# Performance work log

Hardware: AMD Instinct MI355X
Metric: run time of the kernel (lower is better)

Reference implementation:

```python
import jax, jax.numpy as jnp
import numpy as np

EPS = 1e-15
NODE_SIZE = 200000
NUM_TYPES = 4
EMBED_DIM = 128
B = 131072
W_POS = 5
W_NEG = 10


def setup_inputs() -> dict:
    key = jax.random.key(0)
    k1, k2, k3, k4, k5, k6 = jax.random.split(key, 6)
    start_node = jax.random.randint(k1, (B, 1), 0, NODE_SIZE)
    pos_samples = jax.random.randint(k2, (B, W_POS), 0, NODE_SIZE)
    neg_samples = jax.random.randint(k3, (B, W_NEG), 0, NODE_SIZE)
    node_types = jax.random.randint(k4, (NODE_SIZE,), 0, NUM_TYPES).astype(jnp.int32)
    start_embeds = jax.random.normal(k5, (NODE_SIZE, EMBED_DIM), dtype=jnp.float32)
    end_embeds = jax.random.normal(k6, (NODE_SIZE, NUM_TYPES, EMBED_DIM), dtype=jnp.float32)
    return {
        'start_embeds': start_embeds,
        'end_embeds': end_embeds,
        'start_node': start_node,
        'pos_samples': pos_samples,
        'neg_samples': neg_samples,
        'node_types': node_types,
    }


def reference(start_embeds, end_embeds, start_node, pos_samples, neg_samples, node_types):
    # start_node: [B,1]; pos_samples: [B,W]; neg_samples: [B,N]
    start_emb = start_embeds[start_node]            # [B,1,D]
    node_type = node_types[start_node]              # [B,1]
    pos_emb = end_embeds[pos_samples, node_type]    # [B,W,D] (node_type broadcasts over W)
    neg_emb = end_embeds[neg_samples, node_type]    # [B,N,D]
    pos_dot = jnp.sum(start_emb * pos_emb, axis=-1)  # [B,W]
    neg_dot = jnp.sum(start_emb * neg_emb, axis=-1)  # [B,N]
    pos_prob = jax.nn.sigmoid(pos_dot)
    neg_prob = jax.nn.sigmoid(neg_dot)
    loss = (-jnp.mean(jnp.log(pos_prob + EPS), axis=1)
            - jnp.mean(jnp.log(1.0 - neg_prob + EPS), axis=1))  # [B]
    return loss
```

## Files before the change

kernel.cpp:

```cpp
#include <hip/hip_runtime.h>
#include <math.h>

#define EPS 1e-15f
#define D 128
#define NTYPES 4

__global__ __launch_bounds__(256) void mp2v_kernel(
    const float* __restrict__ start_embeds,
    const float* __restrict__ end_embeds,
    const int* __restrict__ start_node,
    const int* __restrict__ pos_samples,
    const int* __restrict__ neg_samples,
    const int* __restrict__ node_types,
    float* __restrict__ out,
    int nrows)
{
    const int lane = threadIdx.x & 63;
    const int half = lane >> 5;
    const int m    = lane & 31;
    const int row  = blockIdx.x * (blockDim.x >> 6) + (threadIdx.x >> 6);
    if (row >= nrows) return;

    const int snode = start_node[row];
    const int t     = node_types[snode];

    int myidx = 0;
    if (lane < 5)        myidx = pos_samples[row * 5 + lane];
    else if (lane < 15)  myidx = neg_samples[row * 10 + (lane - 5)];

    const float4 s4 = ((const float4*)(start_embeds + (size_t)snode * D))[m];

    float4 e4[8];
#pragma unroll
    for (int i = 0; i < 8; ++i) {
        int src = 2 * i + half;
        if (src > 14) src = 14;
        const int idx = __shfl(myidx, src);
        e4[i] = ((const float4*)(end_embeds + ((size_t)idx * NTYPES + t) * D))[m];
    }

    float posAcc = 0.0f, negAcc = 0.0f;
#pragma unroll
    for (int i = 0; i < 8; ++i) {
        const float p0 = __fmul_rn(e4[i].x, s4.x);
        const float p1 = __fmul_rn(e4[i].y, s4.y);
        const float p2 = __fmul_rn(e4[i].z, s4.z);
        const float p3 = __fmul_rn(e4[i].w, s4.w);
        float p = __fadd_rn(__fadd_rn(p0, p1), __fadd_rn(p2, p3));
        p = __fadd_rn(p, __shfl_xor(p, 1));
        p = __fadd_rn(p, __shfl_xor(p, 2));
        p = __fadd_rn(p, __shfl_xor(p, 4));
        p = __fadd_rn(p, __shfl_xor(p, 8));
        p = __fadd_rn(p, __shfl_xor(p, 16));

        const float pr = 1.0f / (1.0f + expf(-p));
        const int  s     = 2 * i + half;
        const bool isPos = (s < 5);
        const bool valid = (s < 15);
        const float arg = isPos ? pr : (1.0f - pr);
        const float lg  = logf(arg + EPS);
        posAcc += (isPos && valid) ? lg : 0.0f;
        negAcc += (!isPos && valid) ? lg : 0.0f;
    }

    posAcc += __shfl_xor(posAcc, 32);
    negAcc += __shfl_xor(negAcc, 32);

    if (lane == 0)
        out[row] = -(posAcc / 5.0f) - (negAcc / 10.0f);
}

extern "C" void kernel_launch(void* const* d_in, const int* in_sizes, int n_in,
                              void* d_out, int out_size, void* d_ws, size_t ws_size,
                              hipStream_t stream) {
    const float* start_embeds = (const float*)d_in[0];
    const float* end_embeds   = (const float*)d_in[1];
    const int*   start_node   = (const int*)d_in[2];
    const int*   pos_samples  = (const int*)d_in[3];
    const int*   neg_samples  = (const int*)d_in[4];
    const int*   node_types   = (const int*)d_in[5];
    float* out = (float*)d_out;

    const int nrows = out_size;
    const int wavesPerBlock = 256 / 64;
    const int blocks = (nrows + wavesPerBlock - 1) / wavesPerBlock;
    mp2v_kernel<<<blocks, 256, 0, stream>>>(start_embeds, end_embeds, start_node,
                                            pos_samples, neg_samples, node_types,
                                            out, nrows);
}
```

Baseline: 642.8 us.

## Make kernel persistent with software-pipelined gathers across rows

New measurement: 653.2 us. No clear change (+1.6%).

```diff
diff --git a/kernel.cpp b/kernel.cpp
--- a/kernel.cpp
+++ b/kernel.cpp
@@ -4,6 +4,8 @@
 #define EPS 1e-15f
 #define D 128
 #define NTYPES 4
+#define WPB 4
+#define NBLOCKS 2048
 
 __global__ __launch_bounds__(256) void mp2v_kernel(
     const float* __restrict__ start_embeds,
@@ -18,56 +20,97 @@
     const int lane = threadIdx.x & 63;
     const int half = lane >> 5;
     const int m    = lane & 31;
-    const int row  = blockIdx.x * (blockDim.x >> 6) + (threadIdx.x >> 6);
-    if (row >= nrows) return;
+    const int wid  = blockIdx.x * WPB + (threadIdx.x >> 6);
+    const int nw   = gridDim.x * WPB;
 
-    const int snode = start_node[row];
-    const int t     = node_types[snode];
+    if (wid >= nrows) return;
+    const int iters = (nrows - 1 - wid) / nw + 1;
 
-    int myidx = 0;
-    if (lane < 5)        myidx = pos_samples[row * 5 + lane];
-    else if (lane < 15)  myidx = neg_samples[row * 10 + (lane - 5)];
+#define ROWN(n) (wid + (n) * nw)
 
-    const float4 s4 = ((const float4*)(start_embeds + (size_t)snode * D))[m];
+#define STAGE_X(n, sn, mi)                                          \
+    {   int r_ = ROWN(n); if (r_ >= nrows) r_ = nrows - 1;          \
+        sn = start_node[r_];                                        \
+        mi = 0;                                                     \
+        if (lane < 5)       mi = pos_samples[r_ * 5 + lane];        \
+        else if (lane < 15) mi = neg_samples[r_ * 10 + (lane - 5)]; }
 
-    float4 e4[8];
-#pragma unroll
-    for (int i = 0; i < 8; ++i) {
-        int src = 2 * i + half;
-        if (src > 14) src = 14;
-        const int idx = __shfl(myidx, src);
-        e4[i] = ((const float4*)(end_embeds + ((size_t)idx * NTYPES + t) * D))[m];
+#define STAGE_Z(sn, mi, tt, e4, s4)                                 \
+    {   s4 = ((const float4*)(start_embeds + (size_t)(sn) * D))[m]; \
+        _Pragma("unroll")                                           \
+        for (int i_ = 0; i_ < 8; ++i_) {                            \
+            int src_ = 2 * i_ + half; if (src_ > 14) src_ = 14;     \
+            const int idx_ = __shfl((mi), src_);                    \
+            e4[i_] = ((const float4*)(end_embeds +                  \
+                     ((size_t)idx_ * NTYPES + (tt)) * D))[m];       \
+        }                                                           }
+
+#define STAGE_C(n, e4, s4)                                          \
+    {   float posAcc = 0.0f, negAcc = 0.0f;                         \
+        _Pragma("unroll")                                           \
+        for (int i_ = 0; i_ < 8; ++i_) {                            \
+            const float p0 = __fmul_rn(e4[i_].x, s4.x);             \
+            const float p1 = __fmul_rn(e4[i_].y, s4.y);             \
+            const float p2 = __fmul_rn(e4[i_].z, s4.z);             \
+            const float p3 = __fmul_rn(e4[i_].w, s4.w);             \
+            float p = __fadd_rn(__fadd_rn(p0, p1), __fadd_rn(p2, p3)); \
+            p = __fadd_rn(p, __shfl_xor(p, 1));                     \
+            p = __fadd_rn(p, __shfl_xor(p, 2));                     \
+            p = __fadd_rn(p, __shfl_xor(p, 4));                     \
+            p = __fadd_rn(p, __shfl_xor(p, 8));                     \
+            p = __fadd_rn(p, __shfl_xor(p, 16));                    \
+            const float pr = 1.0f / (1.0f + expf(-p));              \
+            const int  s_    = 2 * i_ + half;                       \
+            const bool isPos = (s_ < 5);                            \
+            const bool valid = (s_ < 15);                           \
+            const float arg = isPos ? pr : (1.0f - pr);             \
+            const float lg  = logf(arg + EPS);                      \
+            posAcc += (isPos && valid) ? lg : 0.0f;                 \
+            negAcc += (!isPos && valid) ? lg : 0.0f;                \
+        }                                                           \
+        posAcc += __shfl_xor(posAcc, 32);                           \
+        negAcc += __shfl_xor(negAcc, 32);                           \
+        if (lane == 0)                                              \
+            out[ROWN(n)] = -(posAcc / 5.0f) - (negAcc / 10.0f);     }
+
+    int sn0, mi0, t0;
+    int sn1, mi1, t1;
+    int sn2, mi2, t2;
+    int sn3, mi3;
+    float4 eA[8], eB[8];
+    float4 sA, sB;
+
+    STAGE_X(0, sn0, mi0);
+    STAGE_X(1, sn1, mi1);
+    STAGE_X(2, sn2, mi2);
+    t0 = node_types[sn0];
+    t1 = node_types[sn1];
+    STAGE_Z(sn0, mi0, t0, eA, sA);
+
+    int n = 0;
+    for (; n + 1 < iters; n += 2) {
+        STAGE_X(n + 3, sn3, mi3);
+        t2 = node_types[sn2];
+        STAGE_Z(sn1, mi1, t1, eB, sB);
+        STAGE_C(n, eA, sA);
+        sn1 = sn2; mi1 = mi2; t1 = t2;
+        sn2 = sn3; mi2 = mi3;
+
+        STAGE_X(n + 4, sn3, mi3);
+        t2 = node_types[sn2];
+        if (n + 2 < iters) STAGE_Z(sn1, mi1, t1, eA, sA);
+        STAGE_C(n + 1, eB, sB);
+        sn1 = sn2; mi1 = mi2; t1 = t2;
+        sn2 = sn3; mi2 = mi3;
+    }
+    if (n < iters) {
+        STAGE_C(n, eA, sA);
     }
 
-    float posAcc = 0.0f, negAcc = 0.0f;
-#pragma unroll
-    for (int i = 0; i < 8; ++i) {
-        const float p0 = __fmul_rn(e4[i].x, s4.x);
-        const float p1 = __fmul_rn(e4[i].y, s4.y);
-        const float p2 = __fmul_rn(e4[i].z, s4.z);
-        const float p3 = __fmul_rn(e4[i].w, s4.w);
-        float p = __fadd_rn(__fadd_rn(p0, p1), __fadd_rn(p2, p3));
-        p = __fadd_rn(p, __shfl_xor(p, 1));
-        p = __fadd_rn(p, __shfl_xor(p, 2));
-        p = __fadd_rn(p, __shfl_xor(p, 4));
-        p = __fadd_rn(p, __shfl_xor(p, 8));
-        p = __fadd_rn(p, __shfl_xor(p, 16));
-
-        const float pr = 1.0f / (1.0f + expf(-p));
-        const int  s     = 2 * i + half;
-        const bool isPos = (s < 5);
-        const bool valid = (s < 15);
-        const float arg = isPos ? pr : (1.0f - pr);
-        const float lg  = logf(arg + EPS);
-        posAcc += (isPos && valid) ? lg : 0.0f;
-        negAcc += (!isPos && valid) ? lg : 0.0f;
-    }
-
-    posAcc += __shfl_xor(posAcc, 32);
-    negAcc += __shfl_xor(negAcc, 32);
-
-    if (lane == 0)
-        out[row] = -(posAcc / 5.0f) - (negAcc / 10.0f);
+#undef STAGE_C
+#undef STAGE_Z
+#undef STAGE_X
+#undef ROWN
 }
 
 extern "C" void kernel_launch(void* const* d_in, const int* in_sizes, int n_in,
@@ -82,8 +125,8 @@
     float* out = (float*)d_out;
 
     const int nrows = out_size;
-    const int wavesPerBlock = 256 / 64;
-    const int blocks = (nrows + wavesPerBlock - 1) / wavesPerBlock;
+    int blocks = (nrows + WPB - 1) / WPB;
+    if (blocks > NBLOCKS) blocks = NBLOCKS;
     mp2v_kernel<<<blocks, 256, 0, stream>>>(start_embeds, end_embeds, start_node,
                                             pos_samples, neg_samples, node_types,
                                             out, nrows);
```
